# Performance work log

Hardware: AMD Instinct MI355X
Metric: run time of the kernel (lower is better)

Reference implementation:

```python
import jax, jax.numpy as jnp
import numpy as np

B, IMSIZE, D, L, M, H = 8, 128, 64, 1, 16384, 100
N = B * IMSIZE * IMSIZE


def _build_edges(size, length):
    # build_perception: each pixel connects to all pixels within Chebyshev radius `length`
    ii, jj = np.meshgrid(np.arange(size), np.arange(size), indexing='ij')
    src, dst = [], []
    for dx in range(-length, length + 1):
        for dy in range(-length, length + 1):
            ok = (ii + dx >= 0) & (ii + dx < size) & (jj + dy >= 0) & (jj + dy < size)
            src.append((ii * size + jj)[ok])
            dst.append(((ii + dx) * size + (jj + dy))[ok])
    return np.concatenate(src), np.concatenate(dst)


def setup_inputs() -> dict:
    key = jax.random.key(0)
    ks = jax.random.split(key, 12)
    x = jax.random.normal(ks[0], (N, D), jnp.float32)  # RDN pixel features, flattened
    cluster = jax.random.randint(ks[1], (N,), 0, M).astype(jnp.int32)  # affinity-pool assignment
    s, d = _build_edges(IMSIZE, L)
    offs = (np.arange(B) * IMSIZE * IMSIZE)[:, None]
    edge_src = jnp.asarray((s[None] + offs).reshape(-1), jnp.int32)
    edge_dst = jnp.asarray((d[None] + offs).reshape(-1), jnp.int32)
    ii, jj = np.meshgrid(np.arange(IMSIZE), np.arange(IMSIZE), indexing='ij')
    g = np.stack([ii, jj], -1).reshape(-1, 2).astype(np.float32) / IMSIZE
    coords = jnp.asarray(np.tile(g, (B, 1)))  # spatial_coords.repeat(batch, 1)
    init = lambda k, sh: jax.random.normal(k, sh, jnp.float32) * 0.05
    params = dict(
        W1=init(ks[2], (D + 4, H)), b1=jnp.zeros((H,), jnp.float32),
        W2=init(ks[3], (H, H)), b2=jnp.zeros((H,), jnp.float32),
        W3=init(ks[4], (H, D)), b3=jnp.zeros((D,), jnp.float32),
        Wr=init(ks[5], (D, D)), Wn=init(ks[6], (D, D)), bg=jnp.zeros((D,), jnp.float32),
        Q1w=init(ks[7], (D, H)), Q1b=jnp.zeros((H,), jnp.float32),
        Q2w=init(ks[8], (H, H)), Q2b=jnp.zeros((H,), jnp.float32),
        Q3w=init(ks[9], (H, H)), Q3b=jnp.zeros((H,), jnp.float32),
        Q4w=init(ks[10], (H, 18)), Q4b=jnp.zeros((18,), jnp.float32),
    )
    out = dict(x=x, coords=coords, cluster=cluster, edge_src=edge_src, edge_dst=edge_dst)
    out.update(params)
    return out


def _render_qtr(G, feats):
    # RenderQTR, vectorized over the 3 channels: quadratic texture rendering per pixel
    centers, paras = feats[:, :2], feats[:, 2:20].reshape(-1, 3, 6)
    dx = (G[:, 0] - centers[:, 0])[:, None]
    dy = (G[:, 1] - centers[:, 1])[:, None]
    a, ah, aw, ahh, aww, ahw = (paras[:, :, k] for k in range(6))
    return a + ah * dx + aw * dy + ahh * dx * dx + aww * dy * dy + ahw * dx * dy


def reference(x, coords, cluster, edge_src, edge_dst, W1, b1, W2, b2, W3, b3, Wr, Wn, bg, Q1w, Q1b, Q2w, Q2b, Q3w, Q3b, Q4w, Q4b):
    # --- affinity-aggregation pooling (scatter-mean coarsening) ---
    cnt = jnp.maximum(jax.ops.segment_sum(jnp.ones((N, 1), x.dtype), cluster, num_segments=M), 1.0)
    xp = jax.ops.segment_sum(x, cluster, num_segments=M) / cnt
    cent = jax.ops.segment_sum(coords, cluster, num_segments=M) / cnt          # scatter_mean centroids
    mom = jax.ops.segment_sum(coords * coords, cluster, num_segments=M) / cnt  # scatter_mean moments
    # --- node transform FCBlock on [feat, 10*centroid, 10*moment] ---
    h = jnp.concatenate([xp, 10.0 * cent, 10.0 * mom], axis=-1)
    h = jax.nn.relu(h @ W1 + b1)
    h = jax.nn.relu(h @ W2 + b2)
    h = h @ W3 + b3
    # --- GraphConv(aggr='max') on cluster-coarsened edges (index-chase) ---
    cs, cd = cluster[edge_src], cluster[edge_dst]
    agg = jax.ops.segment_max((h @ Wn)[cs], cd, num_segments=M)
    agg = jnp.where(jnp.isfinite(agg), agg, 0.0)  # empty segments -> 0
    feat = h @ Wr + agg + bg
    # --- node_to_qtr_p2 FCBlock -> joint spatial features ---
    q = jax.nn.relu(feat @ Q1w + Q1b)
    q = jax.nn.relu(q @ Q2w + Q2b)
    q = jax.nn.relu(q @ Q3w + Q3b)
    q = q @ Q4w + Q4b
    jsf = jnp.concatenate([q, cent], axis=-1)[cluster]  # un-pool gather back to pixel nodes
    recon = _render_qtr(coords, jsf)                     # [N, 3]
    return recon.reshape(B, IMSIZE * IMSIZE, 3)          # to_dense_batch (equal-size batches)
```

## Files before the change

### kernel.cpp

```cpp
#include <hip/hip_runtime.h>
#include <hip/hip_fp16.h>
#include <cmath>

#define SSZ    128
#define SS     (SSZ*SSZ)
#define NB     8
#define NNODES (NB*SS)
#define DD     64
#define MM     16384
#define HH     100
#define BINCAP 64
#define KP     136
#define WSLOT  (112*KP)

typedef _Float16 f16x8 __attribute__((ext_vector_type(8)));
typedef _Float16 f16x2 __attribute__((ext_vector_type(2)));
typedef float    f32x4 __attribute__((ext_vector_type(4)));

__device__ __forceinline__ f16x2 hmax2(f16x2 a, f16x2 b) {
    f16x2 r;
    r.x = (a.x > b.x) ? a.x : b.x;
    r.y = (a.y > b.y) ? a.y : b.y;
    return r;
}

__global__ void k_prep(const float* __restrict__ W1, const float* __restrict__ W2,
                       const float* __restrict__ W3, const float* __restrict__ Wn,
                       const float* __restrict__ Wr, const float* __restrict__ Q1w,
                       const float* __restrict__ Q2w, const float* __restrict__ Q3w,
                       const float* __restrict__ Q4w, __half* __restrict__ Wt,
                       int* __restrict__ binCnt) {
    int idx = blockIdx.x * 256 + threadIdx.x;
    if (idx < MM) binCnt[idx] = 0;
    if (idx >= 9 * WSLOT) return;
    int mat = idx / WSLOT, rem = idx - mat * WSLOT;
    int n = rem / KP, k = rem - n * KP;
    const float* src; int K, N;
    switch (mat) {
        case 0: src = W1;  K = 68;  N = 100; break;
        case 1: src = W2;  K = 100; N = 100; break;
        case 2: src = W3;  K = 100; N = 64;  break;
        case 3: src = Wn;  K = 64;  N = 64;  break;
        case 4: src = Wr;  K = 64;  N = 64;  break;
        case 5: src = Q1w; K = 64;  N = 100; break;
        case 6: src = Q2w; K = 100; N = 100; break;
        case 7: src = Q3w; K = 100; N = 100; break;
        default:src = Q4w; K = 100; N = 18;  break;
    }
    float v = (n < N && k < K) ? src[k * N + n] : 0.0f;
    Wt[idx] = __float2half(v);
}

__global__ void k_scatter(const int* __restrict__ cluster,
                          int* __restrict__ binCnt, int* __restrict__ nodeList) {
    int n = blockIdx.x * 256 + threadIdx.x;
    if (n >= NNODES) return;
    int c = cluster[n];
    int pos = atomicAdd(&binCnt[c], 1);
    if (pos < BINCAP) nodeList[c * BINCAP + pos] = n;
}

template<int KC, int NT>
__device__ __forceinline__ void mfma_stage(
    const _Float16* __restrict__ inBuf, _Float16* __restrict__ outBuf,
    const _Float16* __restrict__ Wt, const float* __restrict__ bias,
    int Nout, bool relu, int w, int lane) {
    const int m = lane & 15, q = lane >> 4;
    f16x8 a[KC];
    #pragma unroll
    for (int kc = 0; kc < KC; kc++)
        a[kc] = *(const f16x8*)&inBuf[m * KP + kc * 32 + q * 8];
    #pragma unroll
    for (int tt = 0; tt < (NT + 3) / 4; tt++) {
        const int t = w + tt * 4;
        if (t >= NT) break;
        f32x4 acc = {0.0f, 0.0f, 0.0f, 0.0f};
        #pragma unroll
        for (int kc = 0; kc < KC; kc++) {
            f16x8 b = *(const f16x8*)&Wt[(16 * t + m) * KP + kc * 32 + q * 8];
            acc = __builtin_amdgcn_mfma_f32_16x16x32_f16(a[kc], b, acc, 0, 0, 0);
        }
        const int n = 16 * t + m;
        const float bb = (n < Nout) ? bias[n] : 0.0f;
        #pragma unroll
        for (int r = 0; r < 4; r++) {
            float c = acc[r] + bb;
            if (relu) c = fmaxf(c, 0.0f);
            if (n < Nout) outBuf[(q * 4 + r) * KP + n] = (_Float16)c;
        }
    }
}

__global__ __launch_bounds__(256) void k_mlp1(
    const float* __restrict__ x, const float* __restrict__ coords,
    const int* __restrict__ binCnt, const int* __restrict__ nodeList,
    const __half* __restrict__ WtAll,
    const float* __restrict__ b1, const float* __restrict__ b2,
    const float* __restrict__ b3, const float* __restrict__ bg,
    __half* __restrict__ hWnOut, float* __restrict__ featP,
    float* __restrict__ jsf) {
    __shared__ __align__(16) _Float16 sb0[16 * KP];
    __shared__ __align__(16) _Float16 sb1[16 * KP];
    const _Float16* Wt = (const _Float16*)WtAll;
    const int tid = threadIdx.x, lane = tid & 63, w = tid >> 6;
    const int c0 = blockIdx.x * 16;
    const int m = lane & 15, q = lane >> 4;

    #pragma unroll
    for (int cc = 0; cc < 4; cc++) {
        const int ci = w * 4 + cc;
        const int c  = c0 + ci;
        int cnt = binCnt[c];
        if (cnt > BINCAP) cnt = BINCAP;
        int nl = nodeList[c * BINCAP + lane];
        float sx = 0.0f, sc = 0.0f, sm = 0.0f;
        for (int i0 = 0; i0 < cnt; i0 += 8) {
            float v[8], cv[8];
            #pragma unroll
            for (int u = 0; u < 8; u++) {
                int i = i0 + u;
                int n = __shfl(nl, i & 63);
                if (i < cnt) {
                    v[u]  = x[(size_t)n * 64 + lane];
                    cv[u] = (lane < 2) ? coords[n * 2 + lane] : 0.0f;
                } else { v[u] = 0.0f; cv[u] = 0.0f; }
            }
            #pragma unroll
            for (int u = 0; u < 8; u++) {
                sx += v[u]; sc += cv[u]; sm += cv[u] * cv[u];
            }
        }
        float fcnt = fmaxf((float)cnt, 1.0f);
        sb0[ci * KP + lane] = (_Float16)(sx / fcnt);
        if (lane < 2) {
            float cent = sc / fcnt;
            sb0[ci * KP + 64 + lane] = (_Float16)(10.0f * cent);
            sb0[ci * KP + 66 + lane] = (_Float16)(10.0f * sm / fcnt);
            jsf[c * 20 + 18 + lane] = cent;
        }
    }
    for (int i = tid; i < 16 * 68; i += 256) {
        int r = i / 68, k = 68 + (i - r * 68);
        sb0[r * KP + k] = (_Float16)0.0f;
    }
    for (int i = tid; i < 16 * 36; i += 256) {
        int r = i / 36, k = 100 + (i - r * 36);
        sb1[r * KP + k] = (_Float16)0.0f;
    }
    __syncthreads();

    mfma_stage<3, 7>(sb0, sb1, Wt + 0 * WSLOT, b1, 100, true,  w, lane);
    __syncthreads();
    mfma_stage<4, 7>(sb1, sb0, Wt + 1 * WSLOT, b2, 100, true,  w, lane);
    __syncthreads();
    mfma_stage<4, 4>(sb0, sb1, Wt + 2 * WSLOT, b3, 64,  false, w, lane);
    __syncthreads();

    {
        const _Float16* Wnt = Wt + 3 * WSLOT;
        const _Float16* Wrt = Wt + 4 * WSLOT;
        f16x8 a0 = *(const f16x8*)&sb1[m * KP + q * 8];
        f16x8 a1 = *(const f16x8*)&sb1[m * KP + 32 + q * 8];
        const int t = w;
        f16x8 bn0 = *(const f16x8*)&Wnt[(16 * t + m) * KP + q * 8];
        f16x8 bn1 = *(const f16x8*)&Wnt[(16 * t + m) * KP + 32 + q * 8];
        f16x8 br0 = *(const f16x8*)&Wrt[(16 * t + m) * KP + q * 8];
        f16x8 br1 = *(const f16x8*)&Wrt[(16 * t + m) * KP + 32 + q * 8];
        f32x4 an = {0.0f, 0.0f, 0.0f, 0.0f};
        f32x4 ar = {0.0f, 0.0f, 0.0f, 0.0f};
        an = __builtin_amdgcn_mfma_f32_16x16x32_f16(a0, bn0, an, 0, 0, 0);
        an = __builtin_amdgcn_mfma_f32_16x16x32_f16(a1, bn1, an, 0, 0, 0);
        ar = __builtin_amdgcn_mfma_f32_16x16x32_f16(a0, br0, ar, 0, 0, 0);
        ar = __builtin_amdgcn_mfma_f32_16x16x32_f16(a1, br1, ar, 0, 0, 0);
        const int n = 16 * t + m;
        const float bgv = bg[n];
        #pragma unroll
        for (int r = 0; r < 4; r++) {
            int row = c0 + q * 4 + r;
            hWnOut[row * 64 + n] = __float2half(an[r]);
            featP [row * 64 + n] = ar[r] + bgv;
        }
    }
}

__global__ __launch_bounds__(512) void k_hvmax(
    const int* __restrict__ cluster, const __half* __restrict__ hWn,
    __half* __restrict__ vmax) {
    __shared__ f16x2 hm[10][16][32];
    const int w = threadIdx.x >> 6, lane = threadIdx.x & 63;
    const int blk  = blockIdx.x;
    const int b    = blk >> 7;
    const int rem  = blk & 127;
    const int r0   = (rem >> 3) << 3;
    const int j0   = (rem & 7) << 4;
    const int base = b * SS;
    const f16x2 NEGH = {(_Float16)-65504.0f, (_Float16)-65504.0f};

    for (int lr = w; lr < 10; lr += 8) {
        int gi = r0 - 1 + lr;
        if (gi < 0 || gi >= SSZ) {
            if (lane < 32) {
                #pragma unroll
                for (int k = 0; k < 16; k++) hm[lr][k][lane] = NEGH;
            }
        } else {
            int rowbase = base + gi * SSZ;
            int jl = j0 - 1 + lane;
            int cid = 0;
            if (lane < 18 && jl >= 0 && jl < SSZ) cid = cluster[rowbase + jl];
            f16x2 val[18];
            #pragma unroll
            for (int p = 0; p < 18; p++) {
                int jp = j0 - 1 + p;
                int cp = __shfl(cid, p);
                val[p] = NEGH;
                if (lane < 32 && jp >= 0 && jp < SSZ)
                    val[p] = *(const f16x2*)&hWn[(cp << 6) + (lane << 1)];
            }
            if (lane < 32) {
                #pragma unroll
                for (int k = 0; k < 16; k++)
                    hm[lr][k][lane] = hmax2(hmax2(val[k], val[k + 1]), val[k + 2]);
            }
        }
    }
    __syncthreads();

    const int outbase = (base + (r0 + w) * SSZ + j0) << 6;
    if (lane < 32) {
        #pragma unroll
        for (int k = 0; k < 16; k++) {
            f16x2 v = hmax2(hmax2(hm[w][k][lane], hm[w + 1][k][lane]),
                            hm[w + 2][k][lane]);
            *(f16x2*)&vmax[outbase + (k << 6) + (lane << 1)] = v;
        }
    }
}

__global__ __launch_bounds__(256) void k_qmlp(
    const float* __restrict__ featP, const __half* __restrict__ vmax,
    const int* __restrict__ binCnt, const int* __restrict__ nodeList,
    const __half* __restrict__ WtAll,
    const float* __restrict__ Q1b, const float* __restrict__ Q2b,
    const float* __restrict__ Q3b, const float* __restrict__ Q4b,
    float* __restrict__ jsf) {
    __shared__ __align__(16) _Float16 sb0[16 * KP];
    __shared__ __align__(16) _Float16 sb1[16 * KP];
    const _Float16* Wt = (const _Float16*)WtAll;
    const int tid = threadIdx.x, lane = tid & 63, w = tid >> 6;
    const int c0 = blockIdx.x * 16;
    const int m = lane & 15, q = lane >> 4;

    #pragma unroll
    for (int cc = 0; cc < 4; cc++) {
        const int ci = w * 4 + cc;
        const int c  = c0 + ci;
        int cnt = binCnt[c];
        if (cnt > BINCAP) cnt = BINCAP;
        int nl = nodeList[c * BINCAP + lane];
        float mx = -__builtin_inff();
        for (int i0 = 0; i0 < cnt; i0 += 8) {
            float v[8];
            #pragma unroll
            for (int u = 0; u < 8; u++) {
                int i = i0 + u;
                int n = __shfl(nl, i & 63);
                v[u] = (i < cnt) ? __half2float(vmax[((size_t)n << 6) + lane])
                                 : -__builtin_inff();
            }
            #pragma unroll
            for (int u = 0; u < 8; u++) mx = fmaxf(mx, v[u]);
        }
        float agg = (cnt == 0) ? 0.0f : mx;
        sb0[ci * KP + lane] = (_Float16)(featP[(size_t)c * 64 + lane] + agg);
    }
    for (int i = tid; i < 16 * 36; i += 256) {
        int r = i / 36, k = 100 + (i - r * 36);
        sb0[r * KP + k] = (_Float16)0.0f;
    }
    for (int i = tid; i < 16 * 36; i += 256) {
        int r = i / 36, k = 100 + (i - r * 36);
        sb1[r * KP + k] = (_Float16)0.0f;
    }
    __syncthreads();

    mfma_stage<2, 7>(sb0, sb1, Wt + 5 * WSLOT, Q1b, 100, true, w, lane);
    __syncthreads();
    mfma_stage<4, 7>(sb1, sb0, Wt + 6 * WSLOT, Q2b, 100, true, w, lane);
    __syncthreads();
    mfma_stage<4, 7>(sb0, sb1, Wt + 7 * WSLOT, Q3b, 100, true, w, lane);
    __syncthreads();

    if (w < 2) {
        const _Float16* Q4t = Wt + 8 * WSLOT;
        f16x8 a[4];
        #pragma unroll
        for (int kc = 0; kc < 4; kc++)
            a[kc] = *(const f16x8*)&sb1[m * KP + kc * 32 + q * 8];
        const int t = w;
        f32x4 acc = {0.0f, 0.0f, 0.0f, 0.0f};
        #pragma unroll
        for (int kc = 0; kc < 4; kc++) {
            f16x8 b = *(const f16x8*)&Q4t[(16 * t + m) * KP + kc * 32 + q * 8];
            acc = __builtin_amdgcn_mfma_f32_16x16x32_f16(a[kc], b, acc, 0, 0, 0);
        }
        const int n = 16 * t + m;
        if (n < 18) {
            const float bb = Q4b[n];
            #pragma unroll
            for (int r = 0; r < 4; r++)
                jsf[(c0 + q * 4 + r) * 20 + n] = acc[r] + bb;
        }
    }
}

__global__ void k_render(const float* __restrict__ jsf, const int* __restrict__ cluster,
                         const float* __restrict__ coords, float* __restrict__ out) {
    int n = blockIdx.x * 256 + threadIdx.x;
    if (n >= NNODES) return;
    int c = cluster[n];
    const float4* f4 = (const float4*)&jsf[c * 20];
    float fv[20];
    *(float4*)&fv[0]  = f4[0];
    *(float4*)&fv[4]  = f4[1];
    *(float4*)&fv[8]  = f4[2];
    *(float4*)&fv[12] = f4[3];
    *(float4*)&fv[16] = f4[4];
    float gx = coords[n * 2 + 0], gy = coords[n * 2 + 1];
    float dx = gx - fv[0];
    float dy = gy - fv[1];
    #pragma unroll
    for (int r = 0; r < 3; r++) {
        float a   = fv[2 + r * 6 + 0];
        float ah  = fv[2 + r * 6 + 1];
        float aw  = fv[2 + r * 6 + 2];
        float ahh = fv[2 + r * 6 + 3];
        float aww = fv[2 + r * 6 + 4];
        float ahw = fv[2 + r * 6 + 5];
        out[n * 3 + r] = a + ah * dx + aw * dy + ahh * dx * dx + aww * dy * dy + ahw * dx * dy;
    }
}

extern "C" void kernel_launch(void* const* d_in, const int* in_sizes, int n_in,
                              void* d_out, int out_size, void* d_ws, size_t ws_size,
                              hipStream_t stream) {
    const float* x       = (const float*)d_in[0];
    const float* coords  = (const float*)d_in[1];
    const int*   cluster = (const int*)  d_in[2];
    const float* W1  = (const float*)d_in[5];
    const float* b1  = (const float*)d_in[6];
    const float* W2  = (const float*)d_in[7];
    const float* b2  = (const float*)d_in[8];
    const float* W3  = (const float*)d_in[9];
    const float* b3  = (const float*)d_in[10];
    const float* Wr  = (const float*)d_in[11];
    const float* Wn  = (const float*)d_in[12];
    const float* bg  = (const float*)d_in[13];
    const float* Q1w = (const float*)d_in[14];
    const float* Q1b = (const float*)d_in[15];
    const float* Q2w = (const float*)d_in[16];
    const float* Q2b = (const float*)d_in[17];
    const float* Q3w = (const float*)d_in[18];
    const float* Q3b = (const float*)d_in[19];
    const float* Q4w = (const float*)d_in[20];
    const float* Q4b = (const float*)d_in[21];
    float* out = (float*)d_out;

    int*    binCnt   = (int*)d_ws;
    int*    nodeList = binCnt + MM;
    float*  featP    = (float*)(nodeList + MM * BINCAP);
    float*  jsf      = featP + MM * 64;
    __half* hWnH     = (__half*)(jsf + MM * 20);
    __half* vmaxH    = hWnH + MM * 64;
    __half* WtH      = vmaxH + (size_t)NNODES * 64;

    k_prep   <<<(9 * WSLOT + 255) / 256, 256, 0, stream>>>(W1, W2, W3, Wn, Wr,
                                                           Q1w, Q2w, Q3w, Q4w,
                                                           WtH, binCnt);
    k_scatter<<<(NNODES + 255) / 256, 256, 0, stream>>>(cluster, binCnt, nodeList);
    k_mlp1   <<<MM / 16, 256, 0, stream>>>(x, coords, binCnt, nodeList, WtH,
                                           b1, b2, b3, bg, hWnH, featP, jsf);
    k_hvmax  <<<1024, 512, 0, stream>>>(cluster, hWnH, vmaxH);
    k_qmlp   <<<MM / 16, 256, 0, stream>>>(featP, vmaxH, binCnt, nodeList, WtH,
                                           Q1b, Q2b, Q3b, Q4b, jsf);
    k_render <<<(NNODES + 255) / 256, 256, 0, stream>>>(jsf, cluster, coords, out);
}
```

Measured before the change: 181.0 us.

## Fuse all stages into one persistent cooperative kernel with grid syncs

Replaces the six separate launches (weight prep, binning scatter, node MLP, halo max, query MLP, render) with a single cooperative kernel of 512 blocks. The phases are separated by grid.sync() and use grid-stride loops, with shared memory unioned across phases. The aim is to remove per-launch overhead and the idle gaps between kernels. In exchange it adds grid-wide barrier costs and caps each phase's parallelism at the persistent grid, which gives fewer resident waves than the original per-phase launch sizes.

```diff
diff --git a/kernel.cpp b/kernel.cpp
--- a/kernel.cpp
+++ b/kernel.cpp
@@ -1,6 +1,9 @@
 #include <hip/hip_runtime.h>
 #include <hip/hip_fp16.h>
+#include <hip/hip_cooperative_groups.h>
 #include <cmath>
+
+namespace cg = cooperative_groups;
 
 #define SSZ    128
 #define SS     (SSZ*SSZ)
@@ -12,6 +15,7 @@
 #define BINCAP 64
 #define KP     136
 #define WSLOT  (112*KP)
+#define NBLK   512
 
 typedef _Float16 f16x8 __attribute__((ext_vector_type(8)));
 typedef _Float16 f16x2 __attribute__((ext_vector_type(2)));
@@ -24,45 +28,20 @@
     return r;
 }
 
-__global__ void k_prep(const float* __restrict__ W1, const float* __restrict__ W2,
-                       const float* __restrict__ W3, const float* __restrict__ Wn,
-                       const float* __restrict__ Wr, const float* __restrict__ Q1w,
-                       const float* __restrict__ Q2w, const float* __restrict__ Q3w,
-                       const float* __restrict__ Q4w, __half* __restrict__ Wt,
-                       int* __restrict__ binCnt) {
-    int idx = blockIdx.x * 256 + threadIdx.x;
-    if (idx < MM) binCnt[idx] = 0;
-    if (idx >= 9 * WSLOT) return;
-    int mat = idx / WSLOT, rem = idx - mat * WSLOT;
-    int n = rem / KP, k = rem - n * KP;
-    const float* src; int K, N;
-    switch (mat) {
-        case 0: src = W1;  K = 68;  N = 100; break;
-        case 1: src = W2;  K = 100; N = 100; break;
-        case 2: src = W3;  K = 100; N = 64;  break;
-        case 3: src = Wn;  K = 64;  N = 64;  break;
-        case 4: src = Wr;  K = 64;  N = 64;  break;
-        case 5: src = Q1w; K = 64;  N = 100; break;
-        case 6: src = Q2w; K = 100; N = 100; break;
-        case 7: src = Q3w; K = 100; N = 100; break;
-        default:src = Q4w; K = 100; N = 18;  break;
-    }
-    float v = (n < N && k < K) ? src[k * N + n] : 0.0f;
-    Wt[idx] = __float2half(v);
-}
-
-__global__ void k_scatter(const int* __restrict__ cluster,
-                          int* __restrict__ binCnt, int* __restrict__ nodeList) {
-    int n = blockIdx.x * 256 + threadIdx.x;
-    if (n >= NNODES) return;
-    int c = cluster[n];
-    int pos = atomicAdd(&binCnt[c], 1);
-    if (pos < BINCAP) nodeList[c * BINCAP + pos] = n;
-}
+struct Args {
+    const float *x, *coords;
+    const int   *cluster;
+    const float *W1, *b1, *W2, *b2, *W3, *b3, *Wr, *Wn, *bg;
+    const float *Q1w, *Q1b, *Q2w, *Q2b, *Q3w, *Q3b, *Q4w, *Q4b;
+    float       *out;
+    int         *binCnt, *nodeList;
+    float       *featP, *jsf;
+    __half      *hWn, *vmax, *Wt;
+};
 
 template<int KC, int NT>
 __device__ __forceinline__ void mfma_stage(
-    const _Float16* __restrict__ inBuf, _Float16* __restrict__ outBuf,
+    const _Float16* inBuf, _Float16* outBuf,
     const _Float16* __restrict__ Wt, const float* __restrict__ bias,
     int Nout, bool relu, int w, int lane) {
     const int m = lane & 15, q = lane >> 4;
@@ -91,297 +70,320 @@
     }
 }
 
-__global__ __launch_bounds__(256) void k_mlp1(
-    const float* __restrict__ x, const float* __restrict__ coords,
-    const int* __restrict__ binCnt, const int* __restrict__ nodeList,
-    const __half* __restrict__ WtAll,
-    const float* __restrict__ b1, const float* __restrict__ b2,
-    const float* __restrict__ b3, const float* __restrict__ bg,
-    __half* __restrict__ hWnOut, float* __restrict__ featP,
-    float* __restrict__ jsf) {
-    __shared__ __align__(16) _Float16 sb0[16 * KP];
-    __shared__ __align__(16) _Float16 sb1[16 * KP];
-    const _Float16* Wt = (const _Float16*)WtAll;
-    const int tid = threadIdx.x, lane = tid & 63, w = tid >> 6;
-    const int c0 = blockIdx.x * 16;
+union SharedU {
+    struct { _Float16 sb0[16 * KP]; _Float16 sb1[16 * KP]; } mm;
+    f16x2 hm[10][16][32];
+};
+
+__global__ __launch_bounds__(256, 2) void k_main(Args A) {
+    cg::grid_group grid = cg::this_grid();
+    __shared__ __align__(16) SharedU sh;
+    const int tid  = threadIdx.x;
+    const int lane = tid & 63, w = tid >> 6;
+    const int gidx = blockIdx.x * 256 + tid;
     const int m = lane & 15, q = lane >> 4;
 
-    #pragma unroll
-    for (int cc = 0; cc < 4; cc++) {
-        const int ci = w * 4 + cc;
-        const int c  = c0 + ci;
-        int cnt = binCnt[c];
-        if (cnt > BINCAP) cnt = BINCAP;
-        int nl = nodeList[c * BINCAP + lane];
-        float sx = 0.0f, sc = 0.0f, sm = 0.0f;
-        for (int i0 = 0; i0 < cnt; i0 += 8) {
-            float v[8], cv[8];
+    if (gidx < MM) A.binCnt[gidx] = 0;
+    for (int idx = gidx; idx < 9 * WSLOT; idx += NBLK * 256) {
+        int mat = idx / WSLOT, rem = idx - mat * WSLOT;
+        int n = rem / KP, k = rem - n * KP;
+        const float* src; int K, N;
+        switch (mat) {
+            case 0: src = A.W1;  K = 68;  N = 100; break;
+            case 1: src = A.W2;  K = 100; N = 100; break;
+            case 2: src = A.W3;  K = 100; N = 64;  break;
+            case 3: src = A.Wn;  K = 64;  N = 64;  break;
+            case 4: src = A.Wr;  K = 64;  N = 64;  break;
+            case 5: src = A.Q1w; K = 64;  N = 100; break;
+            case 6: src = A.Q2w; K = 100; N = 100; break;
+            case 7: src = A.Q3w; K = 100; N = 100; break;
+            default:src = A.Q4w; K = 100; N = 18;  break;
+        }
+        float v = (n < N && k < K) ? src[k * N + n] : 0.0f;
+        A.Wt[idx] = __float2half(v);
+    }
+    grid.sync();
+
+    {
+        int c = A.cluster[gidx];
+        int pos = atomicAdd(&A.binCnt[c], 1);
+        if (pos < BINCAP) A.nodeList[c * BINCAP + pos] = gidx;
+    }
+    grid.sync();
+
+    _Float16* sb0 = sh.mm.sb0;
+    _Float16* sb1 = sh.mm.sb1;
+    const _Float16* Wt = (const _Float16*)A.Wt;
+    for (int g = blockIdx.x; g < MM / 16; g += NBLK) {
+        const int c0 = g * 16;
+        #pragma unroll
+        for (int cc = 0; cc < 4; cc++) {
+            const int ci = w * 4 + cc;
+            const int c  = c0 + ci;
+            int cnt = A.binCnt[c];
+            if (cnt > BINCAP) cnt = BINCAP;
+            int nl = A.nodeList[c * BINCAP + lane];
+            float sx = 0.0f, sc = 0.0f, sm = 0.0f;
+            for (int i0 = 0; i0 < cnt; i0 += 8) {
+                float v[8], cv[8];
+                #pragma unroll
+                for (int u = 0; u < 8; u++) {
+                    int i = i0 + u;
+                    int n = __shfl(nl, i & 63);
+                    if (i < cnt) {
+                        v[u]  = A.x[(size_t)n * 64 + lane];
+                        cv[u] = (lane < 2) ? A.coords[n * 2 + lane] : 0.0f;
+                    } else { v[u] = 0.0f; cv[u] = 0.0f; }
+                }
+                #pragma unroll
+                for (int u = 0; u < 8; u++) {
+                    sx += v[u]; sc += cv[u]; sm += cv[u] * cv[u];
+                }
+            }
+            float fcnt = fmaxf((float)cnt, 1.0f);
+            sb0[ci * KP + lane] = (_Float16)(sx / fcnt);
+            if (lane < 2) {
+                float cent = sc / fcnt;
+                sb0[ci * KP + 64 + lane] = (_Float16)(10.0f * cent);
+                sb0[ci * KP + 66 + lane] = (_Float16)(10.0f * sm / fcnt);
+                A.jsf[c * 20 + 18 + lane] = cent;
+            }
+        }
+        for (int i = tid; i < 16 * 68; i += 256) {
+            int r = i / 68, k = 68 + (i - r * 68);
+            sb0[r * KP + k] = (_Float16)0.0f;
+        }
+        for (int i = tid; i < 16 * 36; i += 256) {
+            int r = i / 36, k = 100 + (i - r * 36);
+            sb1[r * KP + k] = (_Float16)0.0f;
+        }
+        __syncthreads();
+
+        mfma_stage<3, 7>(sb0, sb1, Wt + 0 * WSLOT, A.b1, 100, true,  w, lane);
+        __syncthreads();
+        mfma_stage<4, 7>(sb1, sb0, Wt + 1 * WSLOT, A.b2, 100, true,  w, lane);
+        __syncthreads();
+        mfma_stage<4, 4>(sb0, sb1, Wt + 2 * WSLOT, A.b3, 64,  false, w, lane);
+        __syncthreads();
+
+        {
+            const _Float16* Wnt = Wt + 3 * WSLOT;
+            const _Float16* Wrt = Wt + 4 * WSLOT;
+            f16x8 a0 = *(const f16x8*)&sb1[m * KP + q * 8];
+            f16x8 a1 = *(const f16x8*)&sb1[m * KP + 32 + q * 8];
+            const int t = w;
+            f16x8 bn0 = *(const f16x8*)&Wnt[(16 * t + m) * KP + q * 8];
+            f16x8 bn1 = *(const f16x8*)&Wnt[(16 * t + m) * KP + 32 + q * 8];
+            f16x8 br0 = *(const f16x8*)&Wrt[(16 * t + m) * KP + q * 8];
+            f16x8 br1 = *(const f16x8*)&Wrt[(16 * t + m) * KP + 32 + q * 8];
+            f32x4 an = {0.0f, 0.0f, 0.0f, 0.0f};
+            f32x4 ar = {0.0f, 0.0f, 0.0f, 0.0f};
+            an = __builtin_amdgcn_mfma_f32_16x16x32_f16(a0, bn0, an, 0, 0, 0);
+            an = __builtin_amdgcn_mfma_f32_16x16x32_f16(a1, bn1, an, 0, 0, 0);
+            ar = __builtin_amdgcn_mfma_f32_16x16x32_f16(a0, br0, ar, 0, 0, 0);
+            ar = __builtin_amdgcn_mfma_f32_16x16x32_f16(a1, br1, ar, 0, 0, 0);
+            const int n = 16 * t + m;
+            const float bgv = A.bg[n];
             #pragma unroll
-            for (int u = 0; u < 8; u++) {
-                int i = i0 + u;
-                int n = __shfl(nl, i & 63);
-                if (i < cnt) {
-                    v[u]  = x[(size_t)n * 64 + lane];
-                    cv[u] = (lane < 2) ? coords[n * 2 + lane] : 0.0f;
-                } else { v[u] = 0.0f; cv[u] = 0.0f; }
-            }
+            for (int r = 0; r < 4; r++) {
+                int row = c0 + q * 4 + r;
+                A.hWn  [row * 64 + n] = __float2half(an[r]);
+                A.featP[row * 64 + n] = ar[r] + bgv;
+            }
+        }
+        __syncthreads();
+    }
+    grid.sync();
+
+    {
+        const f16x2 NEGH = {(_Float16)-65504.0f, (_Float16)-65504.0f};
+        for (int blk = blockIdx.x; blk < 1024; blk += NBLK) {
+            const int b    = blk >> 7;
+            const int rem  = blk & 127;
+            const int r0   = (rem >> 3) << 3;
+            const int j0   = (rem & 7) << 4;
+            const int base = b * SS;
+
+            for (int lr = w; lr < 10; lr += 4) {
+                int gi = r0 - 1 + lr;
+                if (gi < 0 || gi >= SSZ) {
+                    if (lane < 32) {
+                        #pragma unroll
+                        for (int k = 0; k < 16; k++) sh.hm[lr][k][lane] = NEGH;
+                    }
+                } else {
+                    int rowbase = base + gi * SSZ;
+                    int jl = j0 - 1 + lane;
+                    int cid = 0;
+                    if (lane < 18 && jl >= 0 && jl < SSZ)
+                        cid = A.cluster[rowbase + jl];
+                    f16x2 val[18];
+                    #pragma unroll
+                    for (int p = 0; p < 18; p++) {
+                        int jp = j0 - 1 + p;
+                        int cp = __shfl(cid, p);
+                        val[p] = NEGH;
+                        if (lane < 32 && jp >= 0 && jp < SSZ)
+                            val[p] = *(const f16x2*)&A.hWn[(cp << 6) + (lane << 1)];
+                    }
+                    if (lane < 32) {
+                        #pragma unroll
+                        for (int k = 0; k < 16; k++)
+                            sh.hm[lr][k][lane] =
+                                hmax2(hmax2(val[k], val[k + 1]), val[k + 2]);
+                    }
+                }
+            }
+            __syncthreads();
+
+            if (lane < 32) {
+                for (int rr = w; rr < 8; rr += 4) {
+                    const int outbase = (base + (r0 + rr) * SSZ + j0) << 6;
+                    #pragma unroll
+                    for (int k = 0; k < 16; k++) {
+                        f16x2 v = hmax2(hmax2(sh.hm[rr][k][lane],
+                                              sh.hm[rr + 1][k][lane]),
+                                        sh.hm[rr + 2][k][lane]);
+                        *(f16x2*)&A.vmax[outbase + (k << 6) + (lane << 1)] = v;
+                    }
+                }
+            }
+            __syncthreads();
+        }
+    }
+    grid.sync();
+
+    for (int g = blockIdx.x; g < MM / 16; g += NBLK) {
+        const int c0 = g * 16;
+        #pragma unroll
+        for (int cc = 0; cc < 4; cc++) {
+            const int ci = w * 4 + cc;
+            const int c  = c0 + ci;
+            int cnt = A.binCnt[c];
+            if (cnt > BINCAP) cnt = BINCAP;
+            int nl = A.nodeList[c * BINCAP + lane];
+            float mx = -__builtin_inff();
+            for (int i0 = 0; i0 < cnt; i0 += 8) {
+                float v[8];
+                #pragma unroll
+                for (int u = 0; u < 8; u++) {
+                    int i = i0 + u;
+                    int n = __shfl(nl, i & 63);
+                    v[u] = (i < cnt)
+                         ? __half2float(A.vmax[((size_t)n << 6) + lane])
+                         : -__builtin_inff();
+                }
+                #pragma unroll
+                for (int u = 0; u < 8; u++) mx = fmaxf(mx, v[u]);
+            }
+            float agg = (cnt == 0) ? 0.0f : mx;
+            sb0[ci * KP + lane] =
+                (_Float16)(A.featP[(size_t)c * 64 + lane] + agg);
+        }
+        for (int i = tid; i < 16 * 36; i += 256) {
+            int r = i / 36, k = 100 + (i - r * 36);
+            sb0[r * KP + k] = (_Float16)0.0f;
+        }
+        for (int i = tid; i < 16 * 36; i += 256) {
+            int r = i / 36, k = 100 + (i - r * 36);
+            sb1[r * KP + k] = (_Float16)0.0f;
+        }
+        __syncthreads();
+
+        mfma_stage<2, 7>(sb0, sb1, Wt + 5 * WSLOT, A.Q1b, 100, true, w, lane);
+        __syncthreads();
+        mfma_stage<4, 7>(sb1, sb0, Wt + 6 * WSLOT, A.Q2b, 100, true, w, lane);
+        __syncthreads();
+        mfma_stage<4, 7>(sb0, sb1, Wt + 7 * WSLOT, A.Q3b, 100, true, w, lane);
+        __syncthreads();
+
+        if (w < 2) {
+            const _Float16* Q4t = Wt + 8 * WSLOT;
+            f16x8 a[4];
             #pragma unroll
-            for (int u = 0; u < 8; u++) {
-                sx += v[u]; sc += cv[u]; sm += cv[u] * cv[u];
-            }
-        }
-        float fcnt = fmaxf((float)cnt, 1.0f);
-        sb0[ci * KP + lane] = (_Float16)(sx / fcnt);
-        if (lane < 2) {
-            float cent = sc / fcnt;
-            sb0[ci * KP + 64 + lane] = (_Float16)(10.0f * cent);
-            sb0[ci * KP + 66 + lane] = (_Float16)(10.0f * sm / fcnt);
-            jsf[c * 20 + 18 + lane] = cent;
-        }
-    }
-    for (int i = tid; i < 16 * 68; i += 256) {
-        int r = i / 68, k = 68 + (i - r * 68);
-        sb0[r * KP + k] = (_Float16)0.0f;
-    }
-    for (int i = tid; i < 16 * 36; i += 256) {
-        int r = i / 36, k = 100 + (i - r * 36);
-        sb1[r * KP + k] = (_Float16)0.0f;
-    }
-    __syncthreads();
-
-    mfma_stage<3, 7>(sb0, sb1, Wt + 0 * WSLOT, b1, 100, true,  w, lane);
-    __syncthreads();
-    mfma_stage<4, 7>(sb1, sb0, Wt + 1 * WSLOT, b2, 100, true,  w, lane);
-    __syncthreads();
-    mfma_stage<4, 4>(sb0, sb1, Wt + 2 * WSLOT, b3, 64,  false, w, lane);
-    __syncthreads();
+            for (int kc = 0; kc < 4; kc++)
+                a[kc] = *(const f16x8*)&sb1[m * KP + kc * 32 + q * 8];
+            const int t = w;
+            f32x4 acc = {0.0f, 0.0f, 0.0f, 0.0f};
+            #pragma unroll
+            for (int kc = 0; kc < 4; kc++) {
+                f16x8 b = *(const f16x8*)&Q4t[(16 * t + m) * KP + kc * 32 + q * 8];
+                acc = __builtin_amdgcn_mfma_f32_16x16x32_f16(a[kc], b, acc, 0, 0, 0);
+            }
+            const int n = 16 * t + m;
+            if (n < 18) {
+                const float bb = A.Q4b[n];
+                #pragma unroll
+                for (int r = 0; r < 4; r++)
+                    A.jsf[(c0 + q * 4 + r) * 20 + n] = acc[r] + bb;
+            }
+        }
+        __syncthreads();
+    }
+    grid.sync();
 
     {
-        const _Float16* Wnt = Wt + 3 * WSLOT;
-        const _Float16* Wrt = Wt + 4 * WSLOT;
-        f16x8 a0 = *(const f16x8*)&sb1[m * KP + q * 8];
-        f16x8 a1 = *(const f16x8*)&sb1[m * KP + 32 + q * 8];
-        const int t = w;
-        f16x8 bn0 = *(const f16x8*)&Wnt[(16 * t + m) * KP + q * 8];
-        f16x8 bn1 = *(const f16x8*)&Wnt[(16 * t + m) * KP + 32 + q * 8];
-        f16x8 br0 = *(const f16x8*)&Wrt[(16 * t + m) * KP + q * 8];
-        f16x8 br1 = *(const f16x8*)&Wrt[(16 * t + m) * KP + 32 + q * 8];
-        f32x4 an = {0.0f, 0.0f, 0.0f, 0.0f};
-        f32x4 ar = {0.0f, 0.0f, 0.0f, 0.0f};
-        an = __builtin_amdgcn_mfma_f32_16x16x32_f16(a0, bn0, an, 0, 0, 0);
-        an = __builtin_amdgcn_mfma_f32_16x16x32_f16(a1, bn1, an, 0, 0, 0);
-        ar = __builtin_amdgcn_mfma_f32_16x16x32_f16(a0, br0, ar, 0, 0, 0);
-        ar = __builtin_amdgcn_mfma_f32_16x16x32_f16(a1, br1, ar, 0, 0, 0);
-        const int n = 16 * t + m;
-        const float bgv = bg[n];
-        #pragma unroll
-        for (int r = 0; r < 4; r++) {
-            int row = c0 + q * 4 + r;
-            hWnOut[row * 64 + n] = __float2half(an[r]);
-            featP [row * 64 + n] = ar[r] + bgv;
-        }
-    }
-}
-
-__global__ __launch_bounds__(512) void k_hvmax(
-    const int* __restrict__ cluster, const __half* __restrict__ hWn,
-    __half* __restrict__ vmax) {
-    __shared__ f16x2 hm[10][16][32];
-    const int w = threadIdx.x >> 6, lane = threadIdx.x & 63;
-    const int blk  = blockIdx.x;
-    const int b    = blk >> 7;
-    const int rem  = blk & 127;
-    const int r0   = (rem >> 3) << 3;
-    const int j0   = (rem & 7) << 4;
-    const int base = b * SS;
-    const f16x2 NEGH = {(_Float16)-65504.0f, (_Float16)-65504.0f};
-
-    for (int lr = w; lr < 10; lr += 8) {
-        int gi = r0 - 1 + lr;
-        if (gi < 0 || gi >= SSZ) {
-            if (lane < 32) {
-                #pragma unroll
-                for (int k = 0; k < 16; k++) hm[lr][k][lane] = NEGH;
-            }
-        } else {
-            int rowbase = base + gi * SSZ;
-            int jl = j0 - 1 + lane;
-            int cid = 0;
-            if (lane < 18 && jl >= 0 && jl < SSZ) cid = cluster[rowbase + jl];
-            f16x2 val[18];
-            #pragma unroll
-            for (int p = 0; p < 18; p++) {
-                int jp = j0 - 1 + p;
-                int cp = __shfl(cid, p);
-                val[p] = NEGH;
-                if (lane < 32 && jp >= 0 && jp < SSZ)
-                    val[p] = *(const f16x2*)&hWn[(cp << 6) + (lane << 1)];
-            }
-            if (lane < 32) {
-                #pragma unroll
-                for (int k = 0; k < 16; k++)
-                    hm[lr][k][lane] = hmax2(hmax2(val[k], val[k + 1]), val[k + 2]);
-            }
-        }
-    }
-    __syncthreads();
-
-    const int outbase = (base + (r0 + w) * SSZ + j0) << 6;
-    if (lane < 32) {
-        #pragma unroll
-        for (int k = 0; k < 16; k++) {
-            f16x2 v = hmax2(hmax2(hm[w][k][lane], hm[w + 1][k][lane]),
-                            hm[w + 2][k][lane]);
-            *(f16x2*)&vmax[outbase + (k << 6) + (lane << 1)] = v;
-        }
-    }
-}
-
-__global__ __launch_bounds__(256) void k_qmlp(
-    const float* __restrict__ featP, const __half* __restrict__ vmax,
-    const int* __restrict__ binCnt, const int* __restrict__ nodeList,
-    const __half* __restrict__ WtAll,
-    const float* __restrict__ Q1b, const float* __restrict__ Q2b,
-    const float* __restrict__ Q3b, const float* __restrict__ Q4b,
-    float* __restrict__ jsf) {
-    __shared__ __align__(16) _Float16 sb0[16 * KP];
-    __shared__ __align__(16) _Float16 sb1[16 * KP];
-    const _Float16* Wt = (const _Float16*)WtAll;
-    const int tid = threadIdx.x, lane = tid & 63, w = tid >> 6;
-    const int c0 = blockIdx.x * 16;
-    const int m = lane & 15, q = lane >> 4;
-
-    #pragma unroll
-    for (int cc = 0; cc < 4; cc++) {
-        const int ci = w * 4 + cc;
-        const int c  = c0 + ci;
-        int cnt = binCnt[c];
-        if (cnt > BINCAP) cnt = BINCAP;
-        int nl = nodeList[c * BINCAP + lane];
-        float mx = -__builtin_inff();
-        for (int i0 = 0; i0 < cnt; i0 += 8) {
-            float v[8];
-            #pragma unroll
-            for (int u = 0; u < 8; u++) {
-                int i = i0 + u;
-                int n = __shfl(nl, i & 63);
-                v[u] = (i < cnt) ? __half2float(vmax[((size_t)n << 6) + lane])
-                                 : -__builtin_inff();
-            }
-            #pragma unroll
-            for (int u = 0; u < 8; u++) mx = fmaxf(mx, v[u]);
-        }
-        float agg = (cnt == 0) ? 0.0f : mx;
-        sb0[ci * KP + lane] = (_Float16)(featP[(size_t)c * 64 + lane] + agg);
-    }
-    for (int i = tid; i < 16 * 36; i += 256) {
-        int r = i / 36, k = 100 + (i - r * 36);
-        sb0[r * KP + k] = (_Float16)0.0f;
-    }
-    for (int i = tid; i < 16 * 36; i += 256) {
-        int r = i / 36, k = 100 + (i - r * 36);
-        sb1[r * KP + k] = (_Float16)0.0f;
-    }
-    __syncthreads();
-
-    mfma_stage<2, 7>(sb0, sb1, Wt + 5 * WSLOT, Q1b, 100, true, w, lane);
-    __syncthreads();
-    mfma_stage<4, 7>(sb1, sb0, Wt + 6 * WSLOT, Q2b, 100, true, w, lane);
-    __syncthreads();
-    mfma_stage<4, 7>(sb0, sb1, Wt + 7 * WSLOT, Q3b, 100, true, w, lane);
-    __syncthreads();
-
-    if (w < 2) {
-        const _Float16* Q4t = Wt + 8 * WSLOT;
-        f16x8 a[4];
-        #pragma unroll
-        for (int kc = 0; kc < 4; kc++)
-            a[kc] = *(const f16x8*)&sb1[m * KP + kc * 32 + q * 8];
-        const int t = w;
-        f32x4 acc = {0.0f, 0.0f, 0.0f, 0.0f};
-        #pragma unroll
-        for (int kc = 0; kc < 4; kc++) {
-            f16x8 b = *(const f16x8*)&Q4t[(16 * t + m) * KP + kc * 32 + q * 8];
-            acc = __builtin_amdgcn_mfma_f32_16x16x32_f16(a[kc], b, acc, 0, 0, 0);
-        }
-        const int n = 16 * t + m;
-        if (n < 18) {
-            const float bb = Q4b[n];
-            #pragma unroll
-            for (int r = 0; r < 4; r++)
-                jsf[(c0 + q * 4 + r) * 20 + n] = acc[r] + bb;
-        }
-    }
-}
-
-__global__ void k_render(const float* __restrict__ jsf, const int* __restrict__ cluster,
-                         const float* __restrict__ coords, float* __restrict__ out) {
-    int n = blockIdx.x * 256 + threadIdx.x;
-    if (n >= NNODES) return;
-    int c = cluster[n];
-    const float4* f4 = (const float4*)&jsf[c * 20];
-    float fv[20];
-    *(float4*)&fv[0]  = f4[0];
-    *(float4*)&fv[4]  = f4[1];
-    *(float4*)&fv[8]  = f4[2];
-    *(float4*)&fv[12] = f4[3];
-    *(float4*)&fv[16] = f4[4];
-    float gx = coords[n * 2 + 0], gy = coords[n * 2 + 1];
-    float dx = gx - fv[0];
-    float dy = gy - fv[1];
-    #pragma unroll
-    for (int r = 0; r < 3; r++) {
-        float a   = fv[2 + r * 6 + 0];
-        float ah  = fv[2 + r * 6 + 1];
-        float aw  = fv[2 + r * 6 + 2];
-        float ahh = fv[2 + r * 6 + 3];
-        float aww = fv[2 + r * 6 + 4];
-        float ahw = fv[2 + r * 6 + 5];
-        out[n * 3 + r] = a + ah * dx + aw * dy + ahh * dx * dx + aww * dy * dy + ahw * dx * dy;
+        const int n = gidx;
+        int c = A.cluster[n];
+        const float4* f4 = (const float4*)&A.jsf[c * 20];
+        float fv[20];
+        *(float4*)&fv[0]  = f4[0];
+        *(float4*)&fv[4]  = f4[1];
+        *(float4*)&fv[8]  = f4[2];
+        *(float4*)&fv[12] = f4[3];
+        *(float4*)&fv[16] = f4[4];
+        float gx = A.coords[n * 2 + 0], gy = A.coords[n * 2 + 1];
+        float dx = gx - fv[0];
+        float dy = gy - fv[1];
+        #pragma unroll
+        for (int r = 0; r < 3; r++) {
+            float a   = fv[2 + r * 6 + 0];
+            float ah  = fv[2 + r * 6 + 1];
+            float aw  = fv[2 + r * 6 + 2];
+            float ahh = fv[2 + r * 6 + 3];
+            float aww = fv[2 + r * 6 + 4];
+            float ahw = fv[2 + r * 6 + 5];
+            A.out[n * 3 + r] = a + ah * dx + aw * dy + ahh * dx * dx
+                             + aww * dy * dy + ahw * dx * dy;
+        }
     }
 }
 
 extern "C" void kernel_launch(void* const* d_in, const int* in_sizes, int n_in,
                               void* d_out, int out_size, void* d_ws, size_t ws_size,
                               hipStream_t stream) {
-    const float* x       = (const float*)d_in[0];
-    const float* coords  = (const float*)d_in[1];
-    const int*   cluster = (const int*)  d_in[2];
-    const float* W1  = (const float*)d_in[5];
-    const float* b1  = (const float*)d_in[6];
-    const float* W2  = (const float*)d_in[7];
-    const float* b2  = (const float*)d_in[8];
-    const float* W3  = (const float*)d_in[9];
-    const float* b3  = (const float*)d_in[10];
-    const float* Wr  = (const float*)d_in[11];
-    const float* Wn  = (const float*)d_in[12];
-    const float* bg  = (const float*)d_in[13];
-    const float* Q1w = (const float*)d_in[14];
-    const float* Q1b = (const float*)d_in[15];
-    const float* Q2w = (const float*)d_in[16];
-    const float* Q2b = (const float*)d_in[17];
-    const float* Q3w = (const float*)d_in[18];
-    const float* Q3b = (const float*)d_in[19];
-    const float* Q4w = (const float*)d_in[20];
-    const float* Q4b = (const float*)d_in[21];
-    float* out = (float*)d_out;
-
-    int*    binCnt   = (int*)d_ws;
-    int*    nodeList = binCnt + MM;
-    float*  featP    = (float*)(nodeList + MM * BINCAP);
-    float*  jsf      = featP + MM * 64;
-    __half* hWnH     = (__half*)(jsf + MM * 20);
-    __half* vmaxH    = hWnH + MM * 64;
-    __half* WtH      = vmaxH + (size_t)NNODES * 64;
-
-    k_prep   <<<(9 * WSLOT + 255) / 256, 256, 0, stream>>>(W1, W2, W3, Wn, Wr,
-                                                           Q1w, Q2w, Q3w, Q4w,
-                                                           WtH, binCnt);
-    k_scatter<<<(NNODES + 255) / 256, 256, 0, stream>>>(cluster, binCnt, nodeList);
-    k_mlp1   <<<MM / 16, 256, 0, stream>>>(x, coords, binCnt, nodeList, WtH,
-                                           b1, b2, b3, bg, hWnH, featP, jsf);
-    k_hvmax  <<<1024, 512, 0, stream>>>(cluster, hWnH, vmaxH);
-    k_qmlp   <<<MM / 16, 256, 0, stream>>>(featP, vmaxH, binCnt, nodeList, WtH,
-                                           Q1b, Q2b, Q3b, Q4b, jsf);
-    k_render <<<(NNODES + 255) / 256, 256, 0, stream>>>(jsf, cluster, coords, out);
+    Args A;
+    A.x       = (const float*)d_in[0];
+    A.coords  = (const float*)d_in[1];
+    A.cluster = (const int*)  d_in[2];
+    A.W1  = (const float*)d_in[5];
+    A.b1  = (const float*)d_in[6];
+    A.W2  = (const float*)d_in[7];
+    A.b2  = (const float*)d_in[8];
+    A.W3  = (const float*)d_in[9];
+    A.b3  = (const float*)d_in[10];
+    A.Wr  = (const float*)d_in[11];
+    A.Wn  = (const float*)d_in[12];
+    A.bg  = (const float*)d_in[13];
+    A.Q1w = (const float*)d_in[14];
+    A.Q1b = (const float*)d_in[15];
+    A.Q2w = (const float*)d_in[16];
+    A.Q2b = (const float*)d_in[17];
+    A.Q3w = (const float*)d_in[18];
+    A.Q3b = (const float*)d_in[19];
+    A.Q4w = (const float*)d_in[20];
+    A.Q4b = (const float*)d_in[21];
+    A.out = (float*)d_out;
+
+    A.binCnt   = (int*)d_ws;
+    A.nodeList = A.binCnt + MM;
+    A.featP    = (float*)(A.nodeList + MM * BINCAP);
+    A.jsf      = A.featP + MM * 64;
+    A.hWn      = (__half*)(A.jsf + MM * 20);
+    A.vmax     = A.hWn + MM * 64;
+    A.Wt       = A.vmax + (size_t)NNODES * 64;
+
+    void* kp[] = { &A };
+    hipLaunchCooperativeKernel((const void*)k_main, dim3(NBLK), dim3(256),
+                               kp, 0, stream);
 }
```

New measurement: 570.5 us. +215.1%, slower.
